# Kernel tuning notes

Hardware: AMD Instinct MI355X
Metric: run time of the kernel (lower is better)

Reference implementation:

```python
import jax, jax.numpy as jnp
import numpy as np

B, C, O, H, W = 4, 256, 256, 64, 64
KH = KW = 3
KK = KH * KW
PAD = 1  # stride=1, padding=1 -> output spatial == input spatial


def setup_inputs() -> dict:
    key = jax.random.key(0)
    k0, k1, k2, k3 = jax.random.split(key, 4)
    x = jax.random.normal(k0, (B, C, H, W), jnp.float32)
    # offset-predicting conv: small weights -> realistic sub-pixel offsets
    w_off = jax.random.normal(k1, (3 * KK, C, KH, KW), jnp.float32) * 0.01
    b_off = jnp.zeros((3 * KK,), jnp.float32)
    w_def = jax.random.normal(k2, (O, C, KH, KW), jnp.float32) * (1.0 / np.sqrt(C * KK))
    b_def = jax.random.normal(k3, (O,), jnp.float32) * 0.01
    return {"x": x, "w_off": w_off, "b_off": b_off, "w_def": w_def, "b_def": b_def}


def _conv2d(x, w, b):
    y = jax.lax.conv_general_dilated(
        x, w, window_strides=(1, 1), padding=((PAD, PAD), (PAD, PAD)),
        dimension_numbers=("NCHW", "OIHW", "NCHW"))
    return y + b[None, :, None, None]


def _deform_conv2d(x, offsets, mask, w, b):
    # torchvision modulated DeformConv2d, stride=1, pad=1, dilation=1.
    Bx, Cx, Hx, Wx = x.shape
    Ox = w.shape[0]
    # offsets: [B, 2*KK, H, W] with channel 2k = dy, 2k+1 = dx for tap k
    off = offsets.reshape(Bx, KK, 2, Hx, Wx)
    ky, kx = jnp.meshgrid(jnp.arange(KH), jnp.arange(KW), indexing="ij")
    ky = ky.reshape(KK)
    kx = kx.reshape(KK)
    base_y = (ky[:, None, None] - PAD + jnp.arange(Hx)[None, :, None]).astype(x.dtype)  # [KK,H,1]
    base_x = (kx[:, None, None] - PAD + jnp.arange(Wx)[None, None, :]).astype(x.dtype)  # [KK,1,W]
    sy = off[:, :, 0] + base_y  # [B,KK,H,W] sample rows
    sx = off[:, :, 1] + base_x  # [B,KK,H,W] sample cols

    y0 = jnp.floor(sy)
    x0 = jnp.floor(sx)
    ty = sy - y0  # fractional weights (grad flows to offsets through these)
    tx = sx - x0

    x_flat = x.reshape(Bx, Cx, Hx * Wx)
    val = jnp.zeros((Bx, Cx, KK, Hx, Wx), x.dtype)
    for dy in (0, 1):  # 4 bilinear corners (fixed small loop)
        for dx in (0, 1):
            yi = y0.astype(jnp.int32) + dy
            xi = x0.astype(jnp.int32) + dx
            wgt = (ty if dy else 1.0 - ty) * (tx if dx else 1.0 - tx)
            valid = (yi >= 0) & (yi < Hx) & (xi >= 0) & (xi < Wx)  # zero outside
            idx = (jnp.clip(yi, 0, Hx - 1) * Wx + jnp.clip(xi, 0, Wx - 1)).reshape(Bx, 1, -1)
            g = jnp.take_along_axis(x_flat, idx, axis=2).reshape(Bx, Cx, KK, Hx, Wx)
            val = val + g * jnp.where(valid, wgt, 0.0)[:, None]

    val = val * mask.reshape(Bx, 1, KK, Hx, Wx)  # modulation
    out = jnp.einsum("bckhw,ock->bohw", val, w.reshape(Ox, Cx, KK))
    return out + b[None, :, None, None]


def reference(x, w_off, b_off, w_def, b_def):
    pred = _conv2d(x, w_off, b_off)            # [B, 3*KK, H, W]
    offsets = pred[:, : 2 * KK]                # [B, 2*KK, H, W]
    mask = jax.nn.sigmoid(pred[:, 2 * KK:])    # [B, KK, H, W]
    return _deform_conv2d(x, offsets, mask, w_def, b_def)
```

## Files before the change

kernel.cpp:

```cpp
#include <hip/hip_runtime.h>

#define BB 4
#define CCH 256
#define OCH 256
#define HH 64
#define WW 64
#define HWSZ 4096

typedef __bf16 bf16_t;
typedef bf16_t bf16x8 __attribute__((ext_vector_type(8)));
typedef bf16_t bf16x2_t __attribute__((ext_vector_type(2)));
typedef float f32x4 __attribute__((ext_vector_type(4)));

__device__ __forceinline__ unsigned int packbf(float a, float b) {
    bf16x2_t p;
    p.x = (__bf16)a;
    p.y = (__bf16)b;
    return __builtin_bit_cast(unsigned int, p);
}
__device__ __forceinline__ float blo(unsigned int u) { return __uint_as_float(u << 16); }
__device__ __forceinline__ float bhi(unsigned int u) { return __uint_as_float(u & 0xFFFF0000u); }

__device__ __forceinline__ void block_sync() {
    asm volatile("s_waitcnt lgkmcnt(0)" ::: "memory");
    __builtin_amdgcn_s_barrier();
    __builtin_amdgcn_sched_barrier(0);
}

__global__ __launch_bounds__(256) void k_prep(const float* __restrict__ x,
                                              const float* __restrict__ w_off,
                                              const float* __restrict__ w_def,
                                              const float* __restrict__ b_def,
                                              ushort* __restrict__ xT,
                                              ushort* __restrict__ w1F,
                                              ushort* __restrict__ w2F,
                                              float* __restrict__ P,
                                              float* __restrict__ out) {
    int bid = blockIdx.x;
    if (bid < 256) {
        int b = bid >> 6;
        int h = bid & 63;
        int tid = threadIdx.x;
        int wv = tid >> 6;
        int lane = tid & 63;

        __shared__ unsigned int buf[64][130];

        const float* xp = x + ((size_t)b * CCH + wv * 64) * HWSZ + h * WW + lane;
#pragma unroll 8
        for (int i = 0; i < 32; ++i) {
            float a = xp[(size_t)(2 * i) * HWSZ];
            float c = xp[(size_t)(2 * i + 1) * HWSZ];
            buf[lane][wv * 32 + i] = packbf(a, c);
        }
        __syncthreads();

        ushort* dst = xT + ((size_t)(b * 64 + h) * 64) * 256;
#pragma unroll
        for (int r = 0; r < 16; ++r) {
            int idx = tid + r * 256;
            int w = idx >> 6;
            int q = idx & 63;
            uint2 v = *(const uint2*)&buf[w][2 * q];
            *(uint2*)(dst + (size_t)w * 256 + q * 4) = v;
        }
        return;
    }

    int i = (bid - 256) * 256 + threadIdx.x;
    if (i < 73728) {
        int j = i & 7;
        int o = (i >> 3) & 31;
        int cSub = (i >> 8) & 31;
        int k = i >> 13;
        float v = 0.0f;
        if (o < 27) v = w_off[((size_t)o * CCH + cSub * 8 + j) * 9 + k];
        w1F[i] = (ushort)(packbf(v, 0.f) & 0xFFFFu);
        return;
    }
    i -= 73728;
    if (i < 589824) {
        int j = i & 7;
        int o = (i >> 3) & 255;
        int cg = (i >> 11) & 31;
        int k = i >> 16;
        float v = w_def[(size_t)o * 2304 + (cg * 8 + j) * 9 + k];
        w2F[i] = (ushort)(packbf(v, 0.f) & 0xFFFFu);
        return;
    }
    i -= 589824;
    if (i < 110592) {
        ((float4*)P)[i] = make_float4(0.f, 0.f, 0.f, 0.f);
        return;
    }
    i -= 110592;
    if (i < 1048576) {
        float v = b_def[(i >> 10) & 255];
        ((float4*)out)[i] = make_float4(v, v, v, v);
    }
}

__global__ __launch_bounds__(256) void k_pred3(const ushort* __restrict__ xT,
                                               const ushort* __restrict__ w1F,
                                               float* __restrict__ P) {
    int bid = blockIdx.x;
    int L = (bid & 7) * 128 + (bid >> 3);
    int g = L & 3;
    int h = (L >> 2) & 63;
    int b = L >> 8;
    int tid = threadIdx.x;
    int spx  = tid & 63;
    int sgrp = tid >> 6;
    int lane = tid & 63;
    int wv   = tid >> 6;
    int l16  = lane & 15;
    int lq   = lane >> 4;

    __shared__ ushort b_lds[2][4][4][16][8];

    const ushort* xTb = xT + (size_t)b * HWSZ * 256;
    const bf16x8* w1v = (const bf16x8*)w1F;

    f32x4 acc[2];
    acc[0] = (f32x4){0.f, 0.f, 0.f, 0.f};
    acc[1] = (f32x4){0.f, 0.f, 0.f, 0.f};

    auto stageLoad = [&](int t) -> uint4 {
        int cg = 2 * g + (t >= 9);
        int k = t - (t >= 9 ? 9 : 0);
        int y   = h + k / 3 - 1;
        int pxs = spx + k % 3 - 1;
        bool ok = (y >= 0 && y < HH && pxs >= 0 && pxs < WW);
        uint4 v = make_uint4(0u, 0u, 0u, 0u);
        if (ok) v = *(const uint4*)(xTb + (size_t)(y * WW + pxs) * 256 + cg * 32 + sgrp * 8);
        return v;
    };
    auto stageWrite = [&](uint4 v, int buf) {
        *(uint4*)&b_lds[buf][sgrp][spx >> 4][spx & 15][0] = v;
    };

    {
        uint4 g0 = stageLoad(0);
        stageWrite(g0, 0);
    }
    block_sync();

    for (int t = 0; t < 18; ++t) {
        int cur = t & 1;
        uint4 gN;
        if (t < 17) gN = stageLoad(t + 1);
        int cg = 2 * g + (t >= 9);
        int k  = t - (t >= 9 ? 9 : 0);
        int row = k * 32 + cg * 4 + lq;
        bf16x8 a0 = w1v[(size_t)row * 32 + 0 * 16 + l16];
        bf16x8 a1 = w1v[(size_t)row * 32 + 1 * 16 + l16];
        bf16x8 bfrag = *(const bf16x8*)&b_lds[cur][lq][wv][l16][0];
        acc[0] = __builtin_amdgcn_mfma_f32_16x16x32_bf16(a0, bfrag, acc[0], 0, 0, 0);
        acc[1] = __builtin_amdgcn_mfma_f32_16x16x32_bf16(a1, bfrag, acc[1], 0, 0, 0);
        if (t < 17) stageWrite(gN, cur ^ 1);
        block_sync();
    }

#pragma unroll
    for (int mf = 0; mf < 2; ++mf) {
#pragma unroll
        for (int r = 0; r < 4; ++r) {
            int o = mf * 16 + lq * 4 + r;
            if (o < 27) {
                atomicAdd(&P[((size_t)b * 27 + o) * HWSZ + h * WW + wv * 16 + l16],
                          acc[mf][r]);
            }
        }
    }
}

__global__ __launch_bounds__(512, 4) void k_deform9(const ushort* __restrict__ xT,
                                                    const float* __restrict__ P,
                                                    const float* __restrict__ b_off,
                                                    const ushort* __restrict__ w2F,
                                                    float* __restrict__ out) {
    int bid = blockIdx.x;
    int L = (bid & 7) * 64 + (bid >> 3);
    int cs = L & 1;
    int h  = (L >> 1) & 63;
    int b  = L >> 7;
    int tid = threadIdx.x;
    int lane = tid & 63;
    int wv   = tid >> 6;
    int l16  = lane & 15;
    int lq   = lane >> 4;
    int px   = tid >> 3;
    int cl   = tid & 7;

    __shared__ ushort b_lds[2][8][4][16][8];

    const char* xTc = (const char*)xT + (size_t)b * HWSZ * 512 + cs * 256 + cl * 16;
    const bf16x8* w2b = (const bf16x8*)w2F + (size_t)(cs * 16) * 256 + wv * 32 + l16;

    uint4* wdst0 = (uint4*)&b_lds[0][cl][px >> 4][(px & 15) ^ cl][0];
    uint4* wdst1 = (uint4*)&b_lds[1][cl][px >> 4][(px & 15) ^ cl][0];

    f32x4 acc[2][4];
#pragma unroll
    for (int mf = 0; mf < 2; ++mf)
#pragma unroll
        for (int nt = 0; nt < 4; ++nt) acc[mf][nt] = (f32x4){0.f, 0.f, 0.f, 0.f};

    const float* Pb = P + (size_t)b * 27 * HWSZ + h * WW + px;

    float pOy, pOx, pMr, bOy, bOx, bMr;
    float wgt[4];
    const char* aptr[4];

    auto loadP = [&](int k) {
        pOy = Pb[(size_t)(2 * k) * HWSZ];
        pOx = Pb[(size_t)(2 * k + 1) * HWSZ];
        pMr = Pb[(size_t)(18 + k) * HWSZ];
        bOy = b_off[2 * k];
        bOx = b_off[2 * k + 1];
        bMr = b_off[18 + k];
    };
    auto calcDesc = [&](int k) {
        float offy = pOy + bOy;
        float offx = pOx + bOx;
        float m = 1.0f / (1.0f + expf(-(pMr + bMr)));
        float sy = offy + (float)(h + k / 3 - 1);
        float sx = offx + (float)(px + k % 3 - 1);
        float y0f = floorf(sy), x0f = floorf(sx);
        float ty = sy - y0f, tx = sx - x0f;
        int y0 = (int)y0f, x0 = (int)x0f;
#pragma unroll
        for (int dy = 0; dy < 2; ++dy) {
#pragma unroll
            for (int dx = 0; dx < 2; ++dx) {
                int yi = y0 + dy, xi = x0 + dx;
                bool ok = (yi >= 0 && yi < HH && xi >= 0 && xi < WW);
                float wg = (dy ? ty : 1.0f - ty) * (dx ? tx : 1.0f - tx) * m;
                wgt[dy * 2 + dx]  = ok ? wg : 0.0f;
                aptr[dy * 2 + dx] = xTc + (size_t)(ok ? (yi * WW + xi) : 0) * 512;
            }
        }
    };

    uint4 gbA[4], gbB[4];
    float wgtA[4], wgtB[4];
    bf16x8 aA[2][2], aB[2][2];

    auto issueGatherTo = [&](uint4 (&gb)[4], float (&wg)[4], int off) {
#pragma unroll
        for (int c = 0; c < 4; ++c) gb[c] = *(const uint4*)(aptr[c] + off);
#pragma unroll
        for (int c = 0; c < 4; ++c) wg[c] = wgt[c];
    };
    auto combineFrom = [&](const uint4 (&g)[4], const float (&w)[4]) -> uint4 {
        uint4 r;
        {
            float lo = w[0]*blo(g[0].x) + w[1]*blo(g[1].x) + w[2]*blo(g[2].x) + w[3]*blo(g[3].x);
            float hi = w[0]*bhi(g[0].x) + w[1]*bhi(g[1].x) + w[2]*bhi(g[2].x) + w[3]*bhi(g[3].x);
            r.x = packbf(lo, hi);
        }
        {
            float lo = w[0]*blo(g[0].y) + w[1]*blo(g[1].y) + w[2]*blo(g[2].y) + w[3]*blo(g[3].y);
            float hi = w[0]*bhi(g[0].y) + w[1]*bhi(g[1].y) + w[2]*bhi(g[2].y) + w[3]*bhi(g[3].y);
            r.y = packbf(lo, hi);
        }
        {
            float lo = w[0]*blo(g[0].z) + w[1]*blo(g[1].z) + w[2]*blo(g[2].z) + w[3]*blo(g[3].z);
            float hi = w[0]*bhi(g[0].z) + w[1]*bhi(g[1].z) + w[2]*bhi(g[2].z) + w[3]*bhi(g[3].z);
            r.z = packbf(lo, hi);
        }
        {
            float lo = w[0]*blo(g[0].w) + w[1]*blo(g[1].w) + w[2]*blo(g[2].w) + w[3]*blo(g[3].w);
            float hi = w[0]*bhi(g[0].w) + w[1]*bhi(g[1].w) + w[2]*bhi(g[2].w) + w[3]*bhi(g[3].w);
            r.w = packbf(lo, hi);
        }
        return r;
    };
    auto loadATo = [&](bf16x8 (&a)[2][2], int t) {
        size_t base = ((size_t)((t >> 1) * 32 + (t & 1) * 8) + lq) * 256;
#pragma unroll
        for (int g = 0; g < 2; ++g)
#pragma unroll
            for (int mf = 0; mf < 2; ++mf)
                a[mf][g] = w2b[base + (size_t)g * 1024 + mf * 16];
    };

#define MFMA_BODY(BUF, AREG)                                                        \
    do {                                                                            \
        bf16x8 bfr[2][4];                                                           \
        _Pragma("unroll")                                                           \
        for (int g = 0; g < 2; ++g) {                                               \
            int kg = g * 4 + lq;                                                    \
            _Pragma("unroll")                                                       \
            for (int nt = 0; nt < 4; ++nt)                                          \
                bfr[g][nt] = *(const bf16x8*)&b_lds[BUF][kg][nt][l16 ^ kg][0];      \
        }                                                                           \
        _Pragma("unroll")                                                           \
        for (int g = 0; g < 2; ++g)                                                 \
            _Pragma("unroll")                                                       \
            for (int mf = 0; mf < 2; ++mf)                                          \
                _Pragma("unroll")                                                   \
                for (int nt = 0; nt < 4; ++nt)                                      \
                    acc[mf][nt] = __builtin_amdgcn_mfma_f32_16x16x32_bf16(          \
                        AREG[mf][g], bfr[g][nt], acc[mf][nt], 0, 0, 0);             \
    } while (0)

    loadP(0);
    calcDesc(0);
    issueGatherTo(gbA, wgtA, 0);
    issueGatherTo(gbB, wgtB, 128);
    loadP(1);
    loadATo(aA, 0);
    *wdst0 = combineFrom(gbA, wgtA);
    block_sync();

    for (int tp = 0; tp < 9; ++tp) {
        if (tp < 8) {
            calcDesc(tp + 1);
            issueGatherTo(gbA, wgtA, 0);
        }
        loadATo(aB, 2 * tp + 1);
        *wdst1 = combineFrom(gbB, wgtB);
        MFMA_BODY(0, aA);
        block_sync();

        if (tp < 8) {
            issueGatherTo(gbB, wgtB, 128);
            if (tp < 7) loadP(tp + 2);
            loadATo(aA, 2 * tp + 2);
            *wdst0 = combineFrom(gbA, wgtA);
        }
        MFMA_BODY(1, aB);
        block_sync();
    }
#undef MFMA_BODY

#pragma unroll
    for (int mf = 0; mf < 2; ++mf) {
#pragma unroll
        for (int nt = 0; nt < 4; ++nt) {
#pragma unroll
            for (int r = 0; r < 4; ++r) {
                int o = wv * 32 + mf * 16 + lq * 4 + r;
                atomicAdd(&out[((size_t)b * OCH + o) * HWSZ + h * WW + nt * 16 + l16],
                          acc[mf][nt][r]);
            }
        }
    }
}

extern "C" void kernel_launch(void* const* d_in, const int* in_sizes, int n_in,
                              void* d_out, int out_size, void* d_ws, size_t ws_size,
                              hipStream_t stream) {
    const float* x     = (const float*)d_in[0];
    const float* w_off = (const float*)d_in[1];
    const float* b_off = (const float*)d_in[2];
    const float* w_def = (const float*)d_in[3];
    const float* b_def = (const float*)d_in[4];
    float* out = (float*)d_out;

    float*  P   = (float*)d_ws;
    ushort* w1F = (ushort*)(P + (size_t)BB * 27 * HWSZ);
    ushort* w2F = w1F + 73728;
    ushort* xT  = w2F + 589824;

    hipLaunchKernelGGL(k_prep, dim3(7376), dim3(256), 0, stream,
                       x, w_off, w_def, b_def, xT, w1F, w2F, P, out);
    hipLaunchKernelGGL(k_pred3, dim3(1024), dim3(256), 0, stream, xT, w1F, P);
    hipLaunchKernelGGL(k_deform9, dim3(512), dim3(512), 0, stream, xT, P, b_off, w2F, out);
}
```

Before: 95.18 us.

## Split deform kernel channels four ways and simplify its gather pipeline

The deform kernel now splits input channels into four 64-channel slices per block instead of two 128-channel slices, so it launches 1024 blocks rather than 512. Each block handles one 64-channel chunk per tap, and the pipeline is rewritten as a fully unrolled 9-step sequence with a single gather buffer. Occupancy is raised via launch_bounds(512,6), and pointers are replaced with int offsets to cut register use. The cost is twice as many atomicAdd output writes and recomputed offset/mask descriptors per block, which also doubles the P reads.

```diff
diff --git a/kernel.cpp b/kernel.cpp
--- a/kernel.cpp
+++ b/kernel.cpp
@@ -174,16 +174,16 @@
     }
 }
 
-__global__ __launch_bounds__(512, 4) void k_deform9(const ushort* __restrict__ xT,
-                                                    const float* __restrict__ P,
-                                                    const float* __restrict__ b_off,
-                                                    const ushort* __restrict__ w2F,
-                                                    float* __restrict__ out) {
+__global__ __launch_bounds__(512, 6) void k_deform11(const ushort* __restrict__ xT,
+                                                     const float* __restrict__ P,
+                                                     const float* __restrict__ b_off,
+                                                     const ushort* __restrict__ w2F,
+                                                     float* __restrict__ out) {
     int bid = blockIdx.x;
-    int L = (bid & 7) * 64 + (bid >> 3);
-    int cs = L & 1;
-    int h  = (L >> 1) & 63;
-    int b  = L >> 7;
+    int L = (bid & 7) * 128 + (bid >> 3);
+    int cs = L & 3;
+    int h  = (L >> 2) & 63;
+    int b  = L >> 8;
     int tid = threadIdx.x;
     int lane = tid & 63;
     int wv   = tid >> 6;
@@ -194,8 +194,8 @@
 
     __shared__ ushort b_lds[2][8][4][16][8];
 
-    const char* xTc = (const char*)xT + (size_t)b * HWSZ * 512 + cs * 256 + cl * 16;
-    const bf16x8* w2b = (const bf16x8*)w2F + (size_t)(cs * 16) * 256 + wv * 32 + l16;
+    const char* xTc = (const char*)xT + (size_t)b * HWSZ * 512 + cs * 128 + cl * 16;
+    const bf16x8* w2b = (const bf16x8*)w2F + wv * 32 + l16;
 
     uint4* wdst0 = (uint4*)&b_lds[0][cl][px >> 4][(px & 15) ^ cl][0];
     uint4* wdst1 = (uint4*)&b_lds[1][cl][px >> 4][(px & 15) ^ cl][0];
@@ -210,7 +210,7 @@
 
     float pOy, pOx, pMr, bOy, bOx, bMr;
     float wgt[4];
-    const char* aptr[4];
+    int aoff[4];
 
     auto loadP = [&](int k) {
         pOy = Pb[(size_t)(2 * k) * HWSZ];
@@ -237,47 +237,44 @@
                 bool ok = (yi >= 0 && yi < HH && xi >= 0 && xi < WW);
                 float wg = (dy ? ty : 1.0f - ty) * (dx ? tx : 1.0f - tx) * m;
                 wgt[dy * 2 + dx]  = ok ? wg : 0.0f;
-                aptr[dy * 2 + dx] = xTc + (size_t)(ok ? (yi * WW + xi) : 0) * 512;
+                aoff[dy * 2 + dx] = (ok ? (yi * WW + xi) : 0) * 512;
             }
         }
     };
 
-    uint4 gbA[4], gbB[4];
-    float wgtA[4], wgtB[4];
-    bf16x8 aA[2][2], aB[2][2];
-
-    auto issueGatherTo = [&](uint4 (&gb)[4], float (&wg)[4], int off) {
-#pragma unroll
-        for (int c = 0; c < 4; ++c) gb[c] = *(const uint4*)(aptr[c] + off);
-#pragma unroll
-        for (int c = 0; c < 4; ++c) wg[c] = wgt[c];
-    };
-    auto combineFrom = [&](const uint4 (&g)[4], const float (&w)[4]) -> uint4 {
+    uint4 gb[4];
+    auto issueGather = [&]() {
+#pragma unroll
+        for (int c = 0; c < 4; ++c) gb[c] = *(const uint4*)(xTc + aoff[c]);
+    };
+    auto combineGb = [&]() -> uint4 {
         uint4 r;
         {
-            float lo = w[0]*blo(g[0].x) + w[1]*blo(g[1].x) + w[2]*blo(g[2].x) + w[3]*blo(g[3].x);
-            float hi = w[0]*bhi(g[0].x) + w[1]*bhi(g[1].x) + w[2]*bhi(g[2].x) + w[3]*bhi(g[3].x);
+            float lo = wgt[0]*blo(gb[0].x) + wgt[1]*blo(gb[1].x) + wgt[2]*blo(gb[2].x) + wgt[3]*blo(gb[3].x);
+            float hi = wgt[0]*bhi(gb[0].x) + wgt[1]*bhi(gb[1].x) + wgt[2]*bhi(gb[2].x) + wgt[3]*bhi(gb[3].x);
             r.x = packbf(lo, hi);
         }
         {
-            float lo = w[0]*blo(g[0].y) + w[1]*blo(g[1].y) + w[2]*blo(g[2].y) + w[3]*blo(g[3].y);
-            float hi = w[0]*bhi(g[0].y) + w[1]*bhi(g[1].y) + w[2]*bhi(g[2].y) + w[3]*bhi(g[3].y);
+            float lo = wgt[0]*blo(gb[0].y) + wgt[1]*blo(gb[1].y) + wgt[2]*blo(gb[2].y) + wgt[3]*blo(gb[3].y);
+            float hi = wgt[0]*bhi(gb[0].y) + wgt[1]*bhi(gb[1].y) + wgt[2]*bhi(gb[2].y) + wgt[3]*bhi(gb[3].y);
             r.y = packbf(lo, hi);
         }
         {
-            float lo = w[0]*blo(g[0].z) + w[1]*blo(g[1].z) + w[2]*blo(g[2].z) + w[3]*blo(g[3].z);
-            float hi = w[0]*bhi(g[0].z) + w[1]*bhi(g[1].z) + w[2]*bhi(g[2].z) + w[3]*bhi(g[3].z);
+            float lo = wgt[0]*blo(gb[0].z) + wgt[1]*blo(gb[1].z) + wgt[2]*blo(gb[2].z) + wgt[3]*blo(gb[3].z);
+            float hi = wgt[0]*bhi(gb[0].z) + wgt[1]*bhi(gb[1].z) + wgt[2]*bhi(gb[2].z) + wgt[3]*bhi(gb[3].z);
             r.z = packbf(lo, hi);
         }
         {
-            float lo = w[0]*blo(g[0].w) + w[1]*blo(g[1].w) + w[2]*blo(g[2].w) + w[3]*blo(g[3].w);
-            float hi = w[0]*bhi(g[0].w) + w[1]*bhi(g[1].w) + w[2]*bhi(g[2].w) + w[3]*bhi(g[3].w);
+            float lo = wgt[0]*blo(gb[0].w) + wgt[1]*blo(gb[1].w) + wgt[2]*blo(gb[2].w) + wgt[3]*blo(gb[3].w);
+            float hi = wgt[0]*bhi(gb[0].w) + wgt[1]*bhi(gb[1].w) + wgt[2]*bhi(gb[2].w) + wgt[3]*bhi(gb[3].w);
             r.w = packbf(lo, hi);
         }
         return r;
     };
+
+    bf16x8 aA[2][2], aB[2][2];
     auto loadATo = [&](bf16x8 (&a)[2][2], int t) {
-        size_t base = ((size_t)((t >> 1) * 32 + (t & 1) * 8) + lq) * 256;
+        size_t base = ((size_t)(t * 32 + cs * 8) + lq) * 256;
 #pragma unroll
         for (int g = 0; g < 2; ++g)
 #pragma unroll
@@ -305,34 +302,38 @@
                         AREG[mf][g], bfr[g][nt], acc[mf][nt], 0, 0, 0);             \
     } while (0)
 
+#define DEF_BODY(T, CUR, WNXT, ACUR, ANXT)                                          \
+    do {                                                                            \
+        if ((T) < 8) *WNXT = combineGb();                  \
+        if ((T) < 7) { calcDesc((T) + 2); issueGather(); }           \
+        if ((T) < 6) loadP((T) + 3);                                                \
+        if ((T) < 8) loadATo(ANXT, (T) + 1);                                        \
+        MFMA_BODY(CUR, ACUR);                                                       \
+        __syncthreads();                                                            \
+    } while (0)
+
     loadP(0);
     calcDesc(0);
-    issueGatherTo(gbA, wgtA, 0);
-    issueGatherTo(gbB, wgtB, 128);
+    issueGather();
+    loadATo(aA, 0);
     loadP(1);
-    loadATo(aA, 0);
-    *wdst0 = combineFrom(gbA, wgtA);
-    block_sync();
-
-    for (int tp = 0; tp < 9; ++tp) {
-        if (tp < 8) {
-            calcDesc(tp + 1);
-            issueGatherTo(gbA, wgtA, 0);
-        }
-        loadATo(aB, 2 * tp + 1);
-        *wdst1 = combineFrom(gbB, wgtB);
-        MFMA_BODY(0, aA);
-        block_sync();
-
-        if (tp < 8) {
-            issueGatherTo(gbB, wgtB, 128);
-            if (tp < 7) loadP(tp + 2);
-            loadATo(aA, 2 * tp + 2);
-            *wdst0 = combineFrom(gbA, wgtA);
-        }
-        MFMA_BODY(1, aB);
-        block_sync();
-    }
+    *wdst0 = combineGb();
+    calcDesc(1);
+    issueGather();
+    loadP(2);
+    __syncthreads();
+
+    DEF_BODY(0, 0, wdst1, aA, aB);
+    DEF_BODY(1, 1, wdst0, aB, aA);
+    DEF_BODY(2, 0, wdst1, aA, aB);
+    DEF_BODY(3, 1, wdst0, aB, aA);
+    DEF_BODY(4, 0, wdst1, aA, aB);
+    DEF_BODY(5, 1, wdst0, aB, aA);
+    DEF_BODY(6, 0, wdst1, aA, aB);
+    DEF_BODY(7, 1, wdst0, aB, aA);
+    DEF_BODY(8, 0, wdst1, aA, aB);
+
+#undef DEF_BODY
 #undef MFMA_BODY
 
 #pragma unroll
@@ -367,5 +368,5 @@
     hipLaunchKernelGGL(k_prep, dim3(7376), dim3(256), 0, stream,
                        x, w_off, w_def, b_def, xT, w1F, w2F, P, out);
     hipLaunchKernelGGL(k_pred3, dim3(1024), dim3(256), 0, stream, xT, w1F, P);
-    hipLaunchKernelGGL(k_deform9, dim3(512), dim3(512), 0, stream, xT, P, b_off, w2F, out);
-}
+    hipLaunchKernelGGL(k_deform11, dim3(1024), dim3(512), 0, stream, xT, P, b_off, w2F, out);
+}
```

After: 158.5 us. 66.6% more time.

## Retile offset-prediction conv to 2 rows per block and reorder deform MFMA/combine

Applied to the files above, without the earlier changes.

The offset-prediction kernel now uses 512-thread blocks covering two output rows and 64 channels per block, in 9 tap iterations instead of 18, with XOR-swizzled LDS writes to avoid bank conflicts. This halves the number of blocks and barrier steps and increases work per block. In the deform kernel, the MFMA body is moved ahead of the combine/LDS write so the gathers have more time to land. The custom block_sync (explicit lgkmcnt wait plus sched_barrier) is replaced with __syncthreads, which may change how the compiler schedules instructions around the barriers.

```diff
diff --git a/kernel.cpp b/kernel.cpp
--- a/kernel.cpp
+++ b/kernel.cpp
@@ -20,12 +20,6 @@
 }
 __device__ __forceinline__ float blo(unsigned int u) { return __uint_as_float(u << 16); }
 __device__ __forceinline__ float bhi(unsigned int u) { return __uint_as_float(u & 0xFFFF0000u); }
-
-__device__ __forceinline__ void block_sync() {
-    asm volatile("s_waitcnt lgkmcnt(0)" ::: "memory");
-    __builtin_amdgcn_s_barrier();
-    __builtin_amdgcn_sched_barrier(0);
-}
 
 __global__ __launch_bounds__(256) void k_prep(const float* __restrict__ x,
                                               const float* __restrict__ w_off,
@@ -100,81 +94,93 @@
     }
 }
 
-__global__ __launch_bounds__(256) void k_pred3(const ushort* __restrict__ xT,
+__global__ __launch_bounds__(512) void k_pred4(const ushort* __restrict__ xT,
                                                const ushort* __restrict__ w1F,
                                                float* __restrict__ P) {
     int bid = blockIdx.x;
-    int L = (bid & 7) * 128 + (bid >> 3);
-    int g = L & 3;
-    int h = (L >> 2) & 63;
-    int b = L >> 8;
+    int L = (bid & 7) * 64 + (bid >> 3);
+    int cs = L & 3;
+    int hg = (L >> 2) & 31;
+    int b  = L >> 7;
     int tid = threadIdx.x;
-    int spx  = tid & 63;
-    int sgrp = tid >> 6;
     int lane = tid & 63;
     int wv   = tid >> 6;
     int l16  = lane & 15;
     int lq   = lane >> 4;
-
-    __shared__ ushort b_lds[2][4][4][16][8];
-
-    const ushort* xTb = xT + (size_t)b * HWSZ * 256;
+    int spx  = tid >> 3;
+    int cl   = tid & 7;
+
+    __shared__ ushort b_lds[2][8][8][16][8];
+
+    const ushort* xTb = xT + (size_t)b * HWSZ * 256 + cs * 64 + cl * 8;
     const bf16x8* w1v = (const bf16x8*)w1F;
 
     f32x4 acc[2];
     acc[0] = (f32x4){0.f, 0.f, 0.f, 0.f};
     acc[1] = (f32x4){0.f, 0.f, 0.f, 0.f};
 
-    auto stageLoad = [&](int t) -> uint4 {
-        int cg = 2 * g + (t >= 9);
-        int k = t - (t >= 9 ? 9 : 0);
-        int y   = h + k / 3 - 1;
-        int pxs = spx + k % 3 - 1;
-        bool ok = (y >= 0 && y < HH && pxs >= 0 && pxs < WW);
+    auto stageLoad = [&](int k, int tpx) -> uint4 {
+        int row = hg * 2 + (tpx >> 6);
+        int col = tpx & 63;
+        int ys = row + k / 3 - 1;
+        int xs = col + k % 3 - 1;
+        bool ok = (ys >= 0 && ys < HH && xs >= 0 && xs < WW);
         uint4 v = make_uint4(0u, 0u, 0u, 0u);
-        if (ok) v = *(const uint4*)(xTb + (size_t)(y * WW + pxs) * 256 + cg * 32 + sgrp * 8);
+        if (ok) v = *(const uint4*)(xTb + (size_t)(ys * WW + xs) * 256);
         return v;
     };
-    auto stageWrite = [&](uint4 v, int buf) {
-        *(uint4*)&b_lds[buf][sgrp][spx >> 4][spx & 15][0] = v;
+    auto stageWrite = [&](uint4 v, int buf, int tpx) {
+        *(uint4*)&b_lds[buf][cl][tpx >> 4][(tpx & 15) ^ cl][0] = v;
     };
 
     {
-        uint4 g0 = stageLoad(0);
-        stageWrite(g0, 0);
-    }
-    block_sync();
-
-    for (int t = 0; t < 18; ++t) {
+        uint4 v0 = stageLoad(0, spx);
+        uint4 v1 = stageLoad(0, spx + 64);
+        stageWrite(v0, 0, spx);
+        stageWrite(v1, 0, spx + 64);
+    }
+    __syncthreads();
+
+    for (int t = 0; t < 9; ++t) {
         int cur = t & 1;
-        uint4 gN;
-        if (t < 17) gN = stageLoad(t + 1);
-        int cg = 2 * g + (t >= 9);
-        int k  = t - (t >= 9 ? 9 : 0);
-        int row = k * 32 + cg * 4 + lq;
-        bf16x8 a0 = w1v[(size_t)row * 32 + 0 * 16 + l16];
-        bf16x8 a1 = w1v[(size_t)row * 32 + 1 * 16 + l16];
-        bf16x8 bfrag = *(const bf16x8*)&b_lds[cur][lq][wv][l16][0];
-        acc[0] = __builtin_amdgcn_mfma_f32_16x16x32_bf16(a0, bfrag, acc[0], 0, 0, 0);
-        acc[1] = __builtin_amdgcn_mfma_f32_16x16x32_bf16(a1, bfrag, acc[1], 0, 0, 0);
-        if (t < 17) stageWrite(gN, cur ^ 1);
-        block_sync();
-    }
-
+        uint4 n0, n1;
+        if (t < 8) {
+            n0 = stageLoad(t + 1, spx);
+            n1 = stageLoad(t + 1, spx + 64);
+        }
+        bf16x8 a00 = w1v[(size_t)(t * 32 + cs * 8 + 0 * 4 + lq) * 32 + 0 * 16 + l16];
+        bf16x8 a01 = w1v[(size_t)(t * 32 + cs * 8 + 0 * 4 + lq) * 32 + 1 * 16 + l16];
+        bf16x8 a10 = w1v[(size_t)(t * 32 + cs * 8 + 1 * 4 + lq) * 32 + 0 * 16 + l16];
+        bf16x8 a11 = w1v[(size_t)(t * 32 + cs * 8 + 1 * 4 + lq) * 32 + 1 * 16 + l16];
+        bf16x8 b0 = *(const bf16x8*)&b_lds[cur][0 * 4 + lq][wv][l16 ^ (0 * 4 + lq)][0];
+        bf16x8 b1 = *(const bf16x8*)&b_lds[cur][1 * 4 + lq][wv][l16 ^ (1 * 4 + lq)][0];
+        acc[0] = __builtin_amdgcn_mfma_f32_16x16x32_bf16(a00, b0, acc[0], 0, 0, 0);
+        acc[1] = __builtin_amdgcn_mfma_f32_16x16x32_bf16(a01, b0, acc[1], 0, 0, 0);
+        acc[0] = __builtin_amdgcn_mfma_f32_16x16x32_bf16(a10, b1, acc[0], 0, 0, 0);
+        acc[1] = __builtin_amdgcn_mfma_f32_16x16x32_bf16(a11, b1, acc[1], 0, 0, 0);
+        if (t < 8) {
+            stageWrite(n0, cur ^ 1, spx);
+            stageWrite(n1, cur ^ 1, spx + 64);
+        }
+        __syncthreads();
+    }
+
+    int prow = hg * 2 + (wv >> 2);
+    int pcol = (wv & 3) * 16 + l16;
 #pragma unroll
     for (int mf = 0; mf < 2; ++mf) {
 #pragma unroll
         for (int r = 0; r < 4; ++r) {
             int o = mf * 16 + lq * 4 + r;
             if (o < 27) {
-                atomicAdd(&P[((size_t)b * 27 + o) * HWSZ + h * WW + wv * 16 + l16],
+                atomicAdd(&P[((size_t)b * 27 + o) * HWSZ + prow * WW + pcol],
                           acc[mf][r]);
             }
         }
     }
 }
 
-__global__ __launch_bounds__(512, 4) void k_deform9(const ushort* __restrict__ xT,
+__global__ __launch_bounds__(512, 4) void k_deform8(const ushort* __restrict__ xT,
                                                     const float* __restrict__ P,
                                                     const float* __restrict__ b_off,
                                                     const ushort* __restrict__ w2F,
@@ -312,7 +318,7 @@
     loadP(1);
     loadATo(aA, 0);
     *wdst0 = combineFrom(gbA, wgtA);
-    block_sync();
+    __syncthreads();
 
     for (int tp = 0; tp < 9; ++tp) {
         if (tp < 8) {
@@ -320,18 +326,20 @@
             issueGatherTo(gbA, wgtA, 0);
         }
         loadATo(aB, 2 * tp + 1);
+        MFMA_BODY(0, aA);
         *wdst1 = combineFrom(gbB, wgtB);
-        MFMA_BODY(0, aA);
-        block_sync();
+        __syncthreads();
 
         if (tp < 8) {
             issueGatherTo(gbB, wgtB, 128);
             if (tp < 7) loadP(tp + 2);
             loadATo(aA, 2 * tp + 2);
+        }
+        MFMA_BODY(1, aB);
+        if (tp < 8) {
             *wdst0 = combineFrom(gbA, wgtA);
         }
-        MFMA_BODY(1, aB);
-        block_sync();
+        __syncthreads();
     }
 #undef MFMA_BODY
 
@@ -366,6 +374,6 @@
 
     hipLaunchKernelGGL(k_prep, dim3(7376), dim3(256), 0, stream,
                        x, w_off, w_def, b_def, xT, w1F, w2F, P, out);
-    hipLaunchKernelGGL(k_pred3, dim3(1024), dim3(256), 0, stream, xT, w1F, P);
-    hipLaunchKernelGGL(k_deform9, dim3(512), dim3(512), 0, stream, xT, P, b_off, w2F, out);
-}
+    hipLaunchKernelGGL(k_pred4, dim3(512), dim3(512), 0, stream, xT, w1F, P);
+    hipLaunchKernelGGL(k_deform8, dim3(512), dim3(512), 0, stream, xT, P, b_off, w2F, out);
+}
```

After: 82.57 us. -13.2%, faster.
